# Optimization experiments

Measured on AMD Instinct MI355X. Metric: run time of the kernel, lower is better.

Reference implementation:

```python
import jax, jax.numpy as jnp
import numpy as np

N_NODES = 50000
N_EDGES = 1600000
DIM_IN = 128
DIM_OUT = 128
EPS = 1e-10


def setup_inputs() -> dict:
    key = jax.random.key(0)
    k1, k2, k3, k4, k5 = jax.random.split(key, 5)
    feat_in = jax.random.normal(k1, (N_NODES, DIM_IN), dtype=jnp.float32)
    rows = jax.random.randint(k2, (N_EDGES,), 0, N_NODES, dtype=jnp.int32)
    cols = jax.random.randint(k3, (N_EDGES,), 0, N_NODES, dtype=jnp.int32)
    # normalized adjacency values (positive, ~1/deg scale)
    vals = jax.random.uniform(k4, (N_EDGES,), dtype=jnp.float32) / 32.0
    W = jax.random.normal(k5, (DIM_OUT, DIM_IN), dtype=jnp.float32) * 0.05
    b = jnp.zeros((DIM_OUT,), dtype=jnp.float32)
    scale = jnp.ones((DIM_OUT,), dtype=jnp.float32)
    offset = jnp.zeros((DIM_OUT,), dtype=jnp.float32)
    return {"feat_in": feat_in, "rows": rows, "cols": cols, "vals": vals,
            "W": W, "b": b, "scale": scale, "offset": offset}


def reference(feat_in, rows, cols, vals, W, b, scale, offset):
    # torch.sparse.mm(adj_norm, feat_in): gather source features, scale by
    # edge value, scatter-add into destination rows.
    msgs = vals[:, None] * feat_in[cols]                       # [E, D_in]
    feat_aggr = jax.ops.segment_sum(msgs, rows, num_segments=N_NODES)  # [N, D_in]
    # f_lin (nn.Linear): x @ W.T + b
    feat_trans = feat_aggr @ W.T + b                           # [N, D_out]
    # act = ReLU
    a = jax.nn.relu(feat_trans)
    # f_norm: per-row (feature-dim) normalization, biased variance
    mean = jnp.mean(a, axis=1, keepdims=True)
    var = jnp.mean((a - mean) ** 2, axis=1, keepdims=True) + EPS
    feat_out = (a - mean) * scale * jax.lax.rsqrt(var) + offset
    return feat_out
```

## Files before the change

### kernel.cpp

```cpp
#include <hip/hip_runtime.h>

typedef unsigned int uint;
typedef unsigned short ushort;
typedef __attribute__((ext_vector_type(8))) short short8;
typedef __attribute__((ext_vector_type(4))) float floatx4;

#define N_NODES 50000
#define N_EDGES 1600000
#define DIM 128
#define LN_EPS 1e-10f

#define NB2 1564
#define CAP2 1280
#define EPB 6250
#define SB 256
#define FCB 1563
#define CAPR 76

__device__ __forceinline__ uint f2bf(float x) {
    uint u = __float_as_uint(x);
    return (u + 0x7FFFu + ((u >> 16) & 1u)) >> 16;
}

__global__ __launch_bounds__(1024) void prep(
    const float* __restrict__ feat, const float* __restrict__ W,
    const int* __restrict__ rows, const int* __restrict__ cols,
    const float* __restrict__ vals, int* __restrict__ gcnt,
    int2* __restrict__ perm, uint* __restrict__ featb_u,
    ushort* __restrict__ wbf)
{
    __shared__ int  cnt[NB2];
    __shared__ int  gbase[NB2];
    __shared__ int  lbase[NB2];
    __shared__ int  csum[64];
    __shared__ uint stash[EPB];
    __shared__ int2 stageE[EPB];
    const int bx = blockIdx.x;
    const int t  = threadIdx.x;

    if (bx >= SB) {
        int cb = bx - SB;
        if (cb < FCB) {
            int i = cb * 1024 + t;
            if (i < N_NODES * DIM / 4) {
                float4 v = ((const float4*)feat)[i];
                ((uint2*)featb_u)[i] = make_uint2(
                    f2bf(v.x) | (f2bf(v.y) << 16),
                    f2bf(v.z) | (f2bf(v.w) << 16));
            }
        } else {
            for (int idx = t; idx < DIM * DIM; idx += 1024)
                wbf[idx] = (ushort)f2bf(W[idx]);
        }
        return;
    }

    for (int i = t; i < NB2; i += 1024) cnt[i] = 0;
    __syncthreads();
    const int base = bx * EPB;
    for (int k = t; k < EPB; k += 1024) {
        int r = rows[base + k];
        int rank = atomicAdd(&cnt[r >> 5], 1);
        stash[k] = ((uint)rank << 16) | (uint)r;
    }
    __syncthreads();

    for (int i = t; i < NB2; i += 1024) {
        int c = cnt[i];
        gbase[i] = c ? atomicAdd(&gcnt[i], c) : 0;
    }
    if (t < 64) {
        int s = 0;
        for (int j = 0; j < 25; ++j) {
            int idx = t * 25 + j;
            if (idx < NB2) s += cnt[idx];
        }
        csum[t] = s;
    }
    __syncthreads();
    if (t == 0) {
        int s = 0;
        for (int i = 0; i < 64; ++i) { int c = csum[i]; csum[i] = s; s += c; }
    }
    __syncthreads();
    if (t < 64) {
        int run = csum[t];
        for (int j = 0; j < 25; ++j) {
            int idx = t * 25 + j;
            if (idx < NB2) { lbase[idx] = run; run += cnt[idx]; }
        }
    }
    __syncthreads();

    for (int k = t; k < EPB; k += 1024) {
        int e = base + k;
        uint s = stash[k];
        int r = (int)(s & 0xFFFFu);
        int rank = (int)(s >> 16);
        int b = r >> 5;
        int pos = lbase[b] + rank;
        stageE[pos] = make_int2(
            (uint)cols[e] | ((uint)(r & 31) << 16) | ((uint)b << 21),
            __float_as_int(vals[e]));
    }
    __syncthreads();

    for (int j = t; j < EPB; j += 1024) {
        int2 p = stageE[j];
        uint b = ((uint)p.x) >> 21;
        int pos = gbase[b] + (j - lbase[b]);
        if (pos < CAP2)
            perm[(size_t)b * CAP2 + pos] = p;
    }
}

__global__ __launch_bounds__(512, 8) void agg_fused(
    const int2* __restrict__ perm, const int* __restrict__ gcnt,
    const ushort* __restrict__ featb, const ushort* __restrict__ wbf,
    const float* __restrict__ bias, const float* __restrict__ scale,
    const float* __restrict__ offset, float* __restrict__ out)
{
    __shared__ int2 lists[32 * CAPR];
    ushort* rowsbuf = (ushort*)lists;
    float*  Cbuf    = (float*)lists;
    __shared__ int  lcnt[32];

    const int t = threadIdx.x;

    const int q = NB2 >> 3, rr = NB2 & 7;
    const int xcd = blockIdx.x & 7, within = blockIdx.x >> 3;
    const int hb = (xcd < rr ? xcd * (q + 1) : rr * (q + 1) + (xcd - rr) * q) + within;

    if (t < 32) lcnt[t] = 0;
    __syncthreads();

    int n = gcnt[hb];
    if (n > CAP2) n = CAP2;
    const int2* pb = perm + (size_t)hb * CAP2;

    for (int e = t; e < n; e += 512) {
        int2 p = pb[e];
        int rl = (p.x >> 16) & 31;
        int pos = atomicAdd(&lcnt[rl], 1);
        if (pos < CAPR)
            lists[rl * CAPR + pos] = make_int2((p.x & 0xFFFF) << 8, p.y);
    }
    __syncthreads();

    const int lane = t & 63;
    const int wid  = t >> 6;
    const int rb   = wid * 4;
    const char* fbase = (const char*)featb;
    const uint  lane4 = (uint)lane << 2;

    float ax[4], ay[4];
    #pragma unroll
    for (int j = 0; j < 4; ++j) {
        int rl = rb + j;
        int cnt = lcnt[rl];
        if (cnt > CAPR) cnt = CAPR;
        const int2* L = &lists[rl * CAPR];
        float sx = 0.f, sy = 0.f;
        int e = 0;
        for (; e + 7 < cnt; e += 8) {
            int2 p[8]; uint g[8];
            #pragma unroll
            for (int k = 0; k < 8; ++k) p[k] = L[e + k];
            #pragma unroll
            for (int k = 0; k < 8; ++k)
                g[k] = *(const uint*)(fbase + ((uint)p[k].x + lane4));
            #pragma unroll
            for (int k = 0; k < 8; ++k) {
                float v = __int_as_float(p[k].y);
                sx = fmaf(v, __uint_as_float(g[k] << 16), sx);
                sy = fmaf(v, __uint_as_float(g[k] & 0xFFFF0000u), sy);
            }
        }
        for (; e < cnt; ++e) {
            int2 p = L[e];
            uint g = *(const uint*)(fbase + ((uint)p.x + lane4));
            float v = __int_as_float(p.y);
            sx = fmaf(v, __uint_as_float(g << 16), sx);
            sy = fmaf(v, __uint_as_float(g & 0xFFFF0000u), sy);
        }
        ax[j] = sx; ay[j] = sy;
    }
    __syncthreads();

    #pragma unroll
    for (int j = 0; j < 4; ++j) {
        uint pk = f2bf(ax[j]) | (f2bf(ay[j]) << 16);
        *(uint*)&rowsbuf[(rb + j) * 136 + 2 * lane] = pk;
    }
    __syncthreads();

    const int l15  = lane & 15;
    const int quad = lane >> 4;
    const int n0   = wid * 16 + l15;
    const float bb = bias[n0];

    floatx4 acc0 = {0.f, 0.f, 0.f, 0.f};
    floatx4 acc1 = {0.f, 0.f, 0.f, 0.f};
    #pragma unroll
    for (int kt = 0; kt < 4; ++kt) {
        int k0 = kt * 32 + quad * 8;
        short8 af0 = *(const short8*)&rowsbuf[l15 * 136 + k0];
        short8 af1 = *(const short8*)&rowsbuf[(l15 + 16) * 136 + k0];
        short8 bf  = *(const short8*)&wbf[n0 * DIM + k0];
        acc0 = __builtin_amdgcn_mfma_f32_16x16x32_bf16(af0, bf, acc0, 0, 0, 0);
        acc1 = __builtin_amdgcn_mfma_f32_16x16x32_bf16(af1, bf, acc1, 0, 0, 0);
    }
    __syncthreads();

    #pragma unroll
    for (int r = 0; r < 4; ++r) {
        int m = quad * 4 + r;
        Cbuf[m * 132 + n0]        = acc0[r] + bb;
        Cbuf[(m + 16) * 132 + n0] = acc1[r] + bb;
    }
    __syncthreads();

    const float sc0 = scale[lane],  sc1 = scale[lane + 64];
    const float of0 = offset[lane], of1 = offset[lane + 64];

    #pragma unroll
    for (int j = 0; j < 4; ++j) {
        int rl = rb + j;
        int r  = hb * 32 + rl;
        if (r >= N_NODES) continue;
        float A0 = fmaxf(Cbuf[rl * 132 + lane],      0.0f);
        float A1 = fmaxf(Cbuf[rl * 132 + lane + 64], 0.0f);

        float s = A0 + A1;
        #pragma unroll
        for (int off = 32; off >= 1; off >>= 1) s += __shfl_xor(s, off, 64);
        float mean = s * (1.0f / 128.0f);

        float d0 = A0 - mean, d1 = A1 - mean;
        float q2 = d0 * d0 + d1 * d1;
        #pragma unroll
        for (int off = 32; off >= 1; off >>= 1) q2 += __shfl_xor(q2, off, 64);
        float rstd = rsqrtf(q2 * (1.0f / 128.0f) + LN_EPS);

        size_t rowp = (size_t)r * DIM;
        out[rowp + lane]      = d0 * sc0 * rstd + of0;
        out[rowp + lane + 64] = d1 * sc1 * rstd + of1;
    }
}

extern "C" void kernel_launch(void* const* d_in, const int* in_sizes, int n_in,
                              void* d_out, int out_size, void* d_ws, size_t ws_size,
                              hipStream_t stream) {
    const float* feat_in = (const float*)d_in[0];
    const int*   rows    = (const int*)d_in[1];
    const int*   cols    = (const int*)d_in[2];
    const float* vals    = (const float*)d_in[3];
    const float* W       = (const float*)d_in[4];
    const float* bias    = (const float*)d_in[5];
    const float* scale   = (const float*)d_in[6];
    const float* offset  = (const float*)d_in[7];
    float* out = (float*)d_out;

    char* p = (char*)d_ws;
    int2* perm = (int2*)p;                 p += (size_t)NB2 * CAP2 * 8;
    ushort* featb = (ushort*)p;            p += (size_t)N_NODES * DIM * 2;
    ushort* wbf = (ushort*)p;              p += DIM * DIM * 2;
    int*  gcnt = (int*)p;                  p += (size_t)(NB2 + 64) * 4;

    hipMemsetAsync(gcnt, 0, (size_t)NB2 * sizeof(int), stream);

    prep<<<SB + FCB + 1, 1024, 0, stream>>>(feat_in, W, rows, cols, vals,
                                            gcnt, perm, (uint*)featb, wbf);
    agg_fused<<<NB2, 512, 0, stream>>>(perm, gcnt, featb, wbf,
                                       bias, scale, offset, out);
}
```

Measured before the change: 174.9 us.

## Split prep into setup and scatter kernels; widen gather unroll with int4 list loads

The fused prep kernel is split in two. A grid-stride setup kernel converts features and W to bf16 and zeroes the bucket counters, which replaces the memset call. A separate scatter kernel keeps per-edge rank and row in registers instead of a shared-memory stash. The aggregation inner loop now reads two edges per int4 from the shared list and unrolls 12 gathers at a time, with a 4-wide remainder loop, to raise memory-level parallelism. The cost is an extra kernel launch, the loss of overlap between the feature conversion and the scatter work, and higher register pressure in agg_fused.

Measured after the change: 174.9 us. Within noise of the previous version (-0.0%).

```diff
diff --git a/kernel.cpp b/kernel.cpp
--- a/kernel.cpp
+++ b/kernel.cpp
@@ -14,7 +14,6 @@
 #define CAP2 1280
 #define EPB 6250
 #define SB 256
-#define FCB 1563
 #define CAPR 76
 
 __device__ __forceinline__ uint f2bf(float x) {
@@ -22,46 +21,54 @@
     return (u + 0x7FFFu + ((u >> 16) & 1u)) >> 16;
 }
 
-__global__ __launch_bounds__(1024) void prep(
+__global__ __launch_bounds__(256) void setup(
     const float* __restrict__ feat, const float* __restrict__ W,
+    uint* __restrict__ featb_u, ushort* __restrict__ wbf,
+    int* __restrict__ gcnt)
+{
+    const int stride = gridDim.x * 256;
+    if (blockIdx.x == 0)
+        for (int i = threadIdx.x; i < NB2; i += 256) gcnt[i] = 0;
+    for (int i = blockIdx.x * 256 + threadIdx.x; i < N_NODES * DIM / 4; i += stride) {
+        float4 v = ((const float4*)feat)[i];
+        ((uint2*)featb_u)[i] = make_uint2(
+            f2bf(v.x) | (f2bf(v.y) << 16),
+            f2bf(v.z) | (f2bf(v.w) << 16));
+    }
+    for (int i = blockIdx.x * 256 + threadIdx.x; i < DIM * DIM / 4; i += stride) {
+        float4 v = ((const float4*)W)[i];
+        ushort4 o;
+        o.x = (ushort)f2bf(v.x); o.y = (ushort)f2bf(v.y);
+        o.z = (ushort)f2bf(v.z); o.w = (ushort)f2bf(v.w);
+        ((ushort4*)wbf)[i] = o;
+    }
+}
+
+__global__ __launch_bounds__(1024) void scatter(
     const int* __restrict__ rows, const int* __restrict__ cols,
     const float* __restrict__ vals, int* __restrict__ gcnt,
-    int2* __restrict__ perm, uint* __restrict__ featb_u,
-    ushort* __restrict__ wbf)
+    int2* __restrict__ perm)
 {
     __shared__ int  cnt[NB2];
     __shared__ int  gbase[NB2];
     __shared__ int  lbase[NB2];
     __shared__ int  csum[64];
-    __shared__ uint stash[EPB];
     __shared__ int2 stageE[EPB];
     const int bx = blockIdx.x;
     const int t  = threadIdx.x;
 
-    if (bx >= SB) {
-        int cb = bx - SB;
-        if (cb < FCB) {
-            int i = cb * 1024 + t;
-            if (i < N_NODES * DIM / 4) {
-                float4 v = ((const float4*)feat)[i];
-                ((uint2*)featb_u)[i] = make_uint2(
-                    f2bf(v.x) | (f2bf(v.y) << 16),
-                    f2bf(v.z) | (f2bf(v.w) << 16));
-            }
-        } else {
-            for (int idx = t; idx < DIM * DIM; idx += 1024)
-                wbf[idx] = (ushort)f2bf(W[idx]);
-        }
-        return;
-    }
-
     for (int i = t; i < NB2; i += 1024) cnt[i] = 0;
     __syncthreads();
     const int base = bx * EPB;
-    for (int k = t; k < EPB; k += 1024) {
-        int r = rows[base + k];
-        int rank = atomicAdd(&cnt[r >> 5], 1);
-        stash[k] = ((uint)rank << 16) | (uint)r;
+    uint pk[7];
+    #pragma unroll
+    for (int i = 0; i < 7; ++i) {
+        int k = i * 1024 + t;
+        if (k < EPB) {
+            int r = rows[base + k];
+            int rank = atomicAdd(&cnt[r >> 5], 1);
+            pk[i] = ((uint)rank << 16) | (uint)r;
+        }
     }
     __syncthreads();
 
@@ -92,16 +99,19 @@
     }
     __syncthreads();
 
-    for (int k = t; k < EPB; k += 1024) {
-        int e = base + k;
-        uint s = stash[k];
-        int r = (int)(s & 0xFFFFu);
-        int rank = (int)(s >> 16);
-        int b = r >> 5;
-        int pos = lbase[b] + rank;
-        stageE[pos] = make_int2(
-            (uint)cols[e] | ((uint)(r & 31) << 16) | ((uint)b << 21),
-            __float_as_int(vals[e]));
+    #pragma unroll
+    for (int i = 0; i < 7; ++i) {
+        int k = i * 1024 + t;
+        if (k < EPB) {
+            uint s = pk[i];
+            int r = (int)(s & 0xFFFFu);
+            int rank = (int)(s >> 16);
+            int b = r >> 5;
+            int pos = lbase[b] + rank;
+            stageE[pos] = make_int2(
+                (uint)cols[base + k] | ((uint)(r & 31) << 16) | ((uint)b << 21),
+                __float_as_int(vals[base + k]));
+        }
     }
     __syncthreads();
 
@@ -162,18 +172,42 @@
         const int2* L = &lists[rl * CAPR];
         float sx = 0.f, sy = 0.f;
         int e = 0;
-        for (; e + 7 < cnt; e += 8) {
-            int2 p[8]; uint g[8];
-            #pragma unroll
-            for (int k = 0; k < 8; ++k) p[k] = L[e + k];
-            #pragma unroll
-            for (int k = 0; k < 8; ++k)
-                g[k] = *(const uint*)(fbase + ((uint)p[k].x + lane4));
-            #pragma unroll
-            for (int k = 0; k < 8; ++k) {
-                float v = __int_as_float(p[k].y);
-                sx = fmaf(v, __uint_as_float(g[k] << 16), sx);
-                sy = fmaf(v, __uint_as_float(g[k] & 0xFFFF0000u), sy);
+        for (; e + 11 < cnt; e += 12) {
+            int4 q6[6]; uint g[12];
+            #pragma unroll
+            for (int k = 0; k < 6; ++k) q6[k] = *(const int4*)&L[e + 2 * k];
+            #pragma unroll
+            for (int k = 0; k < 6; ++k) {
+                g[2*k]   = *(const uint*)(fbase + ((uint)q6[k].x + lane4));
+                g[2*k+1] = *(const uint*)(fbase + ((uint)q6[k].z + lane4));
+            }
+            #pragma unroll
+            for (int k = 0; k < 6; ++k) {
+                float v0 = __int_as_float(q6[k].y);
+                float v1 = __int_as_float(q6[k].w);
+                sx = fmaf(v0, __uint_as_float(g[2*k] << 16), sx);
+                sy = fmaf(v0, __uint_as_float(g[2*k] & 0xFFFF0000u), sy);
+                sx = fmaf(v1, __uint_as_float(g[2*k+1] << 16), sx);
+                sy = fmaf(v1, __uint_as_float(g[2*k+1] & 0xFFFF0000u), sy);
+            }
+        }
+        for (; e + 3 < cnt; e += 4) {
+            int4 q2[2]; uint g[4];
+            #pragma unroll
+            for (int k = 0; k < 2; ++k) q2[k] = *(const int4*)&L[e + 2 * k];
+            #pragma unroll
+            for (int k = 0; k < 2; ++k) {
+                g[2*k]   = *(const uint*)(fbase + ((uint)q2[k].x + lane4));
+                g[2*k+1] = *(const uint*)(fbase + ((uint)q2[k].z + lane4));
+            }
+            #pragma unroll
+            for (int k = 0; k < 2; ++k) {
+                float v0 = __int_as_float(q2[k].y);
+                float v1 = __int_as_float(q2[k].w);
+                sx = fmaf(v0, __uint_as_float(g[2*k] << 16), sx);
+                sy = fmaf(v0, __uint_as_float(g[2*k] & 0xFFFF0000u), sy);
+                sx = fmaf(v1, __uint_as_float(g[2*k+1] << 16), sx);
+                sy = fmaf(v1, __uint_as_float(g[2*k+1] & 0xFFFF0000u), sy);
             }
         }
         for (; e < cnt; ++e) {
@@ -267,10 +301,8 @@
     ushort* wbf = (ushort*)p;              p += DIM * DIM * 2;
     int*  gcnt = (int*)p;                  p += (size_t)(NB2 + 64) * 4;
 
-    hipMemsetAsync(gcnt, 0, (size_t)NB2 * sizeof(int), stream);
-
-    prep<<<SB + FCB + 1, 1024, 0, stream>>>(feat_in, W, rows, cols, vals,
-                                            gcnt, perm, (uint*)featb, wbf);
+    setup<<<1024, 256, 0, stream>>>(feat_in, W, (uint*)featb, wbf, gcnt);
+    scatter<<<SB, 1024, 0, stream>>>(rows, cols, vals, gcnt, perm);
     agg_fused<<<NB2, 512, 0, stream>>>(perm, gcnt, featb, wbf,
                                        bias, scale, offset, out);
 }
```
